# Kernel tuning notes

Hardware: AMD Instinct MI355X
Metric: run time of the kernel (lower is better)

Reference implementation:

```python
import jax, jax.numpy as jnp
import numpy as np

B, S, D = 128, 512, 768          # batch, seq_len, token_dim
NH, HD = 8, 96                    # num_heads, head_dim = sentence_dim/num_heads
HID = 4 * HD                      # hidden_dim = 384


def setup_inputs() -> dict:
    key = jax.random.key(0)
    ks = jax.random.split(key, 9)
    token_embeddings = jax.random.normal(ks[0], (B, S, D), dtype=jnp.float32)
    # variable-length attention mask (1 for real tokens, 0 for padding)
    lengths = jax.random.randint(ks[1], (B,), S // 2, S + 1)
    attention_mask = (jnp.arange(S)[None, :] < lengths[:, None]).astype(jnp.float32)
    s = 0.02
    P  = jax.random.normal(ks[2], (NH, HD, D),   dtype=jnp.float32) * s
    bP = jnp.zeros((NH, HD), dtype=jnp.float32)
    W1 = jax.random.normal(ks[3], (NH, HID, HD), dtype=jnp.float32) * s
    b1 = jnp.zeros((NH, HID), dtype=jnp.float32)
    W2 = jax.random.normal(ks[4], (NH, HD, HID), dtype=jnp.float32) * s
    b2 = jnp.zeros((NH, HD), dtype=jnp.float32)
    return {"token_embeddings": token_embeddings, "attention_mask": attention_mask,
            "P": P, "bP": bP, "W1": W1, "b1": b1, "W2": W2, "b2": b2}


def reference(token_embeddings, attention_mask, P, bP, W1, b1, W2, b2):
    # per-head projection: H_i = P_i(H)           -> (nh, B, S, HD)
    Hi = jnp.einsum('bsd,ihd->ibsh', token_embeddings, P) + bP[:, None, None, :]
    # scores: W2(relu(W1(H_i)))                   -> (nh, B, S, HD)
    A = jnp.einsum('ibsf,ihf->ibsh',
                   jax.nn.relu(jnp.einsum('ibsh,ifh->ibsf', Hi, W1) + b1[:, None, None, :]),
                   W2) + b2[:, None, None, :]
    # masked softmax over sequence dim (log(mask) adds -inf on padding)
    log_mask = jnp.log(attention_mask)[None, :, :, None]  # (1, B, S, 1)
    A = jax.nn.softmax(A + log_mask, axis=2)
    # weighted sum over tokens                    -> (nh, B, HD)
    v = jnp.sum(Hi * A, axis=2)
    # concat heads: (B, nh*HD) = (B, 768)
    pooled = jnp.transpose(v, (1, 0, 2)).reshape(token_embeddings.shape[0], NH * HD)
    return pooled
```

## Files before the change

### kernel.cpp

```cpp
#include <hip/hip_runtime.h>
#include <stdint.h>


typedef short bf16x8 __attribute__((ext_vector_type(8)));
typedef float f32x4 __attribute__((ext_vector_type(4)));

struct alignas(8) us4 { unsigned short x, y, z, w; };

__device__ __forceinline__ unsigned short f32_to_bf16(float f) {
  union { float f; uint32_t u; } v; v.f = f;
  uint32_t u = v.u;
  uint32_t r = (u + 0x7fffu + ((u >> 16) & 1u)) >> 16;
  return (unsigned short)r;
}

__device__ __forceinline__ float bf16_to_f32(unsigned short h) {
  union { uint32_t u; float f; } v; v.u = ((uint32_t)h) << 16;
  return v.f;
}

__device__ __forceinline__ uint32_t pack_bf16_trunc(float lo, float hi) {
  union { float f; uint32_t u; } a, b; a.f = lo; b.f = hi;
  return __builtin_amdgcn_perm(b.u, a.u, 0x07060302u);
}

__device__ __forceinline__ void g2l16(const unsigned short* g, unsigned short* l) {
  __builtin_amdgcn_global_load_lds((__attribute__((address_space(1))) void*)g,
                                   (__attribute__((address_space(3))) void*)l,
                                   16, 0, 0);
}

__device__ __forceinline__ void stageW(const unsigned short* __restrict__ src,
                                       unsigned short* dst, int w, int lane) {
#pragma unroll
  for (int it = 0; it < 4; ++it)
    g2l16(src + (size_t)((it * 4 + w) * 64 + lane) * 8, &dst[(it * 4 + w) * 512]);
  if (w < 2)
    g2l16(src + (size_t)((16 + w) * 64 + lane) * 8, &dst[(16 + w) * 512]);
}


#define N_X   50331648
#define N_P   589824
#define N_W1  294912
#define N_W2  294912
#define N_HI  50331648


__global__ __launch_bounds__(256) void prep(
    const float* __restrict__ X, const float* __restrict__ P,
    const float* __restrict__ W1, const float* __restrict__ W2,
    unsigned short* __restrict__ Xbf, unsigned short* __restrict__ Pbf,
    unsigned short* __restrict__ W1bf, unsigned short* __restrict__ W2bf) {
  const int bx = blockIdx.x;
  const int tid = threadIdx.x;
  if (bx < 49152) {
    const int idx = bx * 256 + tid;
    float4 v = ((const float4*)X)[idx];
    us4 o = {f32_to_bf16(v.x), f32_to_bf16(v.y), f32_to_bf16(v.z), f32_to_bf16(v.w)};
    ((us4*)Xbf)[idx] = o;
  } else if (bx < 49728) {
    const int idx = (bx - 49152) * 256 + tid;
    float4 v = ((const float4*)P)[idx];
    us4 o = {f32_to_bf16(v.x), f32_to_bf16(v.y), f32_to_bf16(v.z), f32_to_bf16(v.w)};
    ((us4*)Pbf)[idx] = o;
  } else if (bx < 49760) {
    const int quarter = bx - 49728;
    const int hd = quarter >> 2, ph = quarter & 3;
    for (int t = tid; t < 1152; t += 256) {
      const int kb = t / 384;
      const int rem = t - kb * 384;
      const int f = rem >> 2, slot = rem & 3;
      const int pos = slot ^ ((f >> 1) & 3);
      const float* src =
          W1 + ((size_t)(hd * 384 + ph * 96 + f)) * 96 + kb * 32 + pos * 8;
      float4 a = *(const float4*)src;
      float4 b = *(const float4*)(src + 4);
      us4 o1 = {f32_to_bf16(a.x), f32_to_bf16(a.y), f32_to_bf16(a.z), f32_to_bf16(a.w)};
      us4 o2 = {f32_to_bf16(b.x), f32_to_bf16(b.y), f32_to_bf16(b.z), f32_to_bf16(b.w)};
      us4* dst = (us4*)(W1bf + (size_t)quarter * 9216 + t * 8);
      dst[0] = o1;
      dst[1] = o2;
    }
  } else {
    const int quarter = bx - 49760;
    const int hd = quarter >> 2, ph = quarter & 3;
    for (int t = tid; t < 1152; t += 256) {
      const int kb = t / 384;
      const int rem = t - kb * 384;
      const int h = rem >> 2, slot = rem & 3;
      const int pos = slot ^ ((h >> 1) & 3);
      const float* src =
          W2 + ((size_t)(hd * 96 + h)) * 384 + ph * 96 + kb * 32 + pos * 8;
      float4 a = *(const float4*)src;
      float4 b = *(const float4*)(src + 4);
      us4 o1 = {f32_to_bf16(a.x), f32_to_bf16(a.y), f32_to_bf16(a.z), f32_to_bf16(a.w)};
      us4 o2 = {f32_to_bf16(b.x), f32_to_bf16(b.y), f32_to_bf16(b.z), f32_to_bf16(b.w)};
      us4* dst = (us4*)(W2bf + (size_t)quarter * 9216 + t * 8);
      dst[0] = o1;
      dst[1] = o2;
    }
  }
}


__global__ __launch_bounds__(256) void gemm_hi(
    const unsigned short* __restrict__ Xbf,
    const unsigned short* __restrict__ Pbf,
    const float* __restrict__ bP,
    unsigned short* __restrict__ Hi) {
  __shared__ __align__(16) unsigned short As[128 * 32];
  __shared__ __align__(16) unsigned short Bs[128 * 32];

  const int tid = threadIdx.x;
  const int w = tid >> 6;
  const int lane = tid & 63;
  const int r = lane & 15;
  const int q = lane >> 4;

  const int hwid = blockIdx.x;
  const int wkid = (hwid & 7) * 384 + (hwid >> 3);
  const int bn = wkid % 6;
  const int bm = wkid / 6;

  const int wr = w >> 1, wc = w & 1;
  const int psw = q ^ ((r >> 1) & 3);

  f32x4 acc[4][4];
#pragma unroll
  for (int a = 0; a < 4; ++a)
#pragma unroll
    for (int c = 0; c < 4; ++c) acc[a][c] = (f32x4){0.f, 0.f, 0.f, 0.f};

  const int ldr = lane >> 2;
  const int ldc = ((lane & 3) ^ ((lane >> 3) & 3)) * 8;
  const unsigned short* Abase = Xbf + (size_t)(bm * 128) * 768 + ldc;
  const unsigned short* Bbase = Pbf + (size_t)(bn * 128) * 768 + ldc;

  for (int k0 = 0; k0 < 768; k0 += 32) {
    __syncthreads();
    g2l16(Abase + (size_t)(w * 16 + ldr) * 768 + k0, &As[w * 512]);
    g2l16(Abase + (size_t)(64 + w * 16 + ldr) * 768 + k0, &As[(4 + w) * 512]);
    g2l16(Bbase + (size_t)(w * 16 + ldr) * 768 + k0, &Bs[w * 512]);
    g2l16(Bbase + (size_t)(64 + w * 16 + ldr) * 768 + k0, &Bs[(4 + w) * 512]);
    __syncthreads();

    bf16x8 af[4], bfr[4];
#pragma unroll
    for (int t = 0; t < 4; ++t)
      af[t] = *(const bf16x8*)&As[(wr * 64 + t * 16 + r) * 32 + psw * 8];
#pragma unroll
    for (int t = 0; t < 4; ++t)
      bfr[t] = *(const bf16x8*)&Bs[(wc * 64 + t * 16 + r) * 32 + psw * 8];
#pragma unroll
    for (int mt = 0; mt < 4; ++mt)
#pragma unroll
      for (int nt = 0; nt < 4; ++nt)
        acc[mt][nt] = __builtin_amdgcn_mfma_f32_16x16x32_bf16(
            af[mt], bfr[nt], acc[mt][nt], 0, 0, 0);
  }

  const int bb = bm >> 2;
  const int sb = (bm & 3) * 128 + wr * 64;
#pragma unroll
  for (int nt = 0; nt < 4; ++nt) {
    const int n0 = bn * 128 + wc * 64 + nt * 16;
    const int hd = n0 / 96;
    const int hloc = n0 - hd * 96;
    const int kb = hloc >> 5;
    const int col = (hloc & 31) + r;
    const float bias = bP[n0 + r];
    unsigned short* obase =
        Hi + (size_t)(hd * 128 + bb) * 49152 + kb * 16384 + col;
#pragma unroll
    for (int mt = 0; mt < 4; ++mt) {
#pragma unroll
      for (int rg = 0; rg < 4; ++rg) {
        const int s = sb + mt * 16 + q * 4 + rg;
        obase[(size_t)s * 32] = f32_to_bf16(acc[mt][nt][rg] + bias);
      }
    }
  }
}


__global__ __launch_bounds__(256, 3) void mlp_pool(
    const unsigned short* __restrict__ Hi,
    const unsigned short* __restrict__ W1bf,
    const unsigned short* __restrict__ W2bf,
    const float* __restrict__ b1,
    const float* __restrict__ b2,
    const float* __restrict__ mask,
    float* __restrict__ out) {
  __shared__ __align__(16) unsigned short U[128 * 104];
  __shared__ __align__(16) unsigned short Ws2[3 * 96 * 32];
  __shared__ __align__(16) float b1s[384];
  __shared__ __align__(16) float b2s[96];
  __shared__ float bias_s[512];
  __shared__ float redA[4][96];
  __shared__ float redB[4][96];

  const int x = blockIdx.x;
  const int b = x & 127;
  const int hd = x >> 7;

  const int tid = threadIdx.x;
  const int w = tid >> 6;
  const int lane = tid & 63;
  const int r = lane & 15;
  const int q = lane >> 4;
  const int psw = q ^ ((r >> 1) & 3);

  if (tid < 96) b2s[tid] = b2[hd * 96 + tid];
  for (int i = tid; i < 384; i += 256) b1s[i] = b1[hd * 384 + i];
  for (int s = tid; s < 512; s += 256)
    bias_s[s] = mask[b * 512 + s] > 0.5f ? 0.f : -1e30f;

  float m_run[6], l_run[6], v_run[6];
#pragma unroll
  for (int nt = 0; nt < 6; ++nt) { m_run[nt] = -3e30f; l_run[nt] = 0.f; v_run[nt] = 0.f; }

  const unsigned short* ysrc = Hi + (size_t)(hd * 128 + b) * 49152;
  const unsigned short* w1h = W1bf + (size_t)(hd * 4) * 9216;
  const unsigned short* w2h = W2bf + (size_t)(hd * 4) * 9216;

  for (int c = 0; c < 4; ++c) {
    const unsigned short* yc = ysrc + c * 4096;

    f32x4 acc3[2][6];
#pragma unroll
    for (int sp = 0; sp < 2; ++sp)
#pragma unroll
      for (int nt = 0; nt < 6; ++nt) acc3[sp][nt] = (f32x4){0.f, 0.f, 0.f, 0.f};

    for (int ph = 0; ph < 4; ++ph) {
      if (c | ph) __syncthreads();
      stageW(w1h + ph * 9216, U, w, lane);
      stageW(w2h + ph * 9216, Ws2, w, lane);
      __syncthreads();

      f32x4 acc2[6][2];
#pragma unroll
      for (int ft = 0; ft < 6; ++ft)
#pragma unroll
        for (int sp = 0; sp < 2; ++sp) acc2[ft][sp] = (f32x4){0.f, 0.f, 0.f, 0.f};
#pragma unroll
      for (int kb = 0; kb < 3; ++kb) {
        bf16x8 bfrg[2];
#pragma unroll
        for (int sp = 0; sp < 2; ++sp)
          bfrg[sp] = *(const bf16x8*)(yc + kb * 16384 +
                                      ((w * 2 + sp) * 16 + r) * 32 + q * 8);
#pragma unroll
        for (int ft = 0; ft < 6; ++ft) {
          bf16x8 afrg = *(const bf16x8*)&U[kb * 3072 + (ft * 16 + r) * 32 + psw * 8];
#pragma unroll
          for (int sp = 0; sp < 2; ++sp)
            acc2[ft][sp] = __builtin_amdgcn_mfma_f32_16x16x32_bf16(
                afrg, bfrg[sp], acc2[ft][sp], 0, 0, 0);
        }
      }
      __syncthreads();

#pragma unroll
      for (int ft = 0; ft < 6; ++ft) {
        float4 bv = *(const float4*)&b1s[ph * 96 + ft * 16 + q * 4];
#pragma unroll
        for (int sp = 0; sp < 2; ++sp) {
          const int s = (w * 2 + sp) * 16 + r;
          float v0 = fmaxf(acc2[ft][sp][0] + bv.x, 0.f);
          float v1 = fmaxf(acc2[ft][sp][1] + bv.y, 0.f);
          float v2 = fmaxf(acc2[ft][sp][2] + bv.z, 0.f);
          float v3 = fmaxf(acc2[ft][sp][3] + bv.w, 0.f);
          uint2 pk;
          pk.x = pack_bf16_trunc(v0, v1);
          pk.y = pack_bf16_trunc(v2, v3);
          *(uint2*)((uint32_t*)&U[0] + s * 52 + ft * 8 + q * 2) = pk;
        }
      }
      __syncthreads();

#pragma unroll
      for (int kb = 0; kb < 3; ++kb) {
        bf16x8 afrg[2];
#pragma unroll
        for (int sp = 0; sp < 2; ++sp)
          afrg[sp] = *(const bf16x8*)&U[((w * 2 + sp) * 16 + r) * 104 + kb * 32 + q * 8];
#pragma unroll
        for (int nt = 0; nt < 6; ++nt) {
          bf16x8 bfrg2 = *(const bf16x8*)&Ws2[kb * 3072 + (nt * 16 + r) * 32 + psw * 8];
#pragma unroll
          for (int sp = 0; sp < 2; ++sp)
            acc3[sp][nt] = __builtin_amdgcn_mfma_f32_16x16x32_bf16(
                afrg[sp], bfrg2, acc3[sp][nt], 0, 0, 0);
        }
      }
    }

#pragma unroll
    for (int nt = 0; nt < 6; ++nt) {
      const float b2v = b2s[nt * 16 + r];
      float lm = -3e30f;
#pragma unroll
      for (int sp = 0; sp < 2; ++sp) {
#pragma unroll
        for (int rg = 0; rg < 4; ++rg) {
          const int sl = (w * 2 + sp) * 16 + q * 4 + rg;
          float lg = acc3[sp][nt][rg] + b2v + bias_s[c * 128 + sl];
          lm = fmaxf(lm, lg);
        }
      }
      lm = fmaxf(lm, __shfl_xor(lm, 16));
      lm = fmaxf(lm, __shfl_xor(lm, 32));
      if (q == 0) redA[w][nt * 16 + r] = lm;
    }
    __syncthreads();
#pragma unroll
    for (int nt = 0; nt < 6; ++nt) {
      const int h = nt * 16 + r;
      const unsigned short* yb = yc + (nt >> 1) * 16384 + (nt & 1) * 16 + r;
      const float cm = fmaxf(fmaxf(redA[0][h], redA[1][h]),
                             fmaxf(redA[2][h], redA[3][h]));
      const float mnew = fmaxf(m_run[nt], cm);
      const float sc = __expf(m_run[nt] - mnew);
      m_run[nt] = mnew;
      float lacc = l_run[nt] * sc;
      float vacc = v_run[nt] * sc;
      const float b2v = b2s[h];
#pragma unroll
      for (int sp = 0; sp < 2; ++sp) {
#pragma unroll
        for (int rg = 0; rg < 4; ++rg) {
          const int sl = (w * 2 + sp) * 16 + q * 4 + rg;
          float lg = acc3[sp][nt][rg] + b2v + bias_s[c * 128 + sl];
          float e = __expf(lg - mnew);
          lacc += e;
          vacc += e * bf16_to_f32(yb[(size_t)sl * 32]);
        }
      }
      l_run[nt] = lacc;
      v_run[nt] = vacc;
    }
  }

  __syncthreads();
#pragma unroll
  for (int nt = 0; nt < 6; ++nt) {
    float ls = l_run[nt], vs = v_run[nt];
    ls += __shfl_xor(ls, 16);
    vs += __shfl_xor(vs, 16);
    ls += __shfl_xor(ls, 32);
    vs += __shfl_xor(vs, 32);
    if (q == 0) {
      redA[w][nt * 16 + r] = ls;
      redB[w][nt * 16 + r] = vs;
    }
  }
  __syncthreads();
  if (tid < 96) {
    float ls = redA[0][tid] + redA[1][tid] + redA[2][tid] + redA[3][tid];
    float vs = redB[0][tid] + redB[1][tid] + redB[2][tid] + redB[3][tid];
    out[(size_t)b * 768 + hd * 96 + tid] = vs / ls;
  }
}


extern "C" void kernel_launch(void* const* d_in, const int* in_sizes, int n_in,
                              void* d_out, int out_size, void* d_ws, size_t ws_size,
                              hipStream_t stream) {
  const float* X    = (const float*)d_in[0];
  const float* mask = (const float*)d_in[1];
  const float* P    = (const float*)d_in[2];
  const float* bP   = (const float*)d_in[3];
  const float* W1   = (const float*)d_in[4];
  const float* b1   = (const float*)d_in[5];
  const float* W2   = (const float*)d_in[6];
  const float* b2   = (const float*)d_in[7];
  float* out = (float*)d_out;
  (void)in_sizes; (void)n_in; (void)out_size; (void)ws_size;

  unsigned short* Xbf  = (unsigned short*)d_ws;
  unsigned short* Pbf  = Xbf + N_X;
  unsigned short* W1bf = Pbf + N_P;
  unsigned short* W2bf = W1bf + N_W1;
  unsigned short* Hi   = W2bf + N_W2;

  prep<<<49792, 256, 0, stream>>>(X, P, W1, W2, Xbf, Pbf, W1bf, W2bf);
  gemm_hi<<<3072, 256, 0, stream>>>(Xbf, Pbf, bP, Hi);
  mlp_pool<<<8 * 128, 256, 0, stream>>>(Hi, W1bf, W2bf, b1, b2, mask, out);
}
```

Before: 591.6 us.

## Stage Hi tiles in LDS and pass relu activations via lane shuffles

The token-chunk tile of Hi is loaded once per chunk into a swizzled LDS buffer, using async global-to-LDS copies. The first GEMM and the weighted value sum then read it from LDS rather than issuing scattered global loads. The intermediate relu activations are repacked into MFMA A-fragments with cross-lane shuffles instead of a round trip through shared memory. W1 and W2 now share one LDS buffer, staged one after the other with an extra barrier. Occupancy drops from 3 to 2 blocks per CU in exchange for more registers.

```diff
diff --git a/kernel.cpp b/kernel.cpp
--- a/kernel.cpp
+++ b/kernel.cpp
@@ -184,7 +184,7 @@
 }
 
 
-__global__ __launch_bounds__(256, 3) void mlp_pool(
+__global__ __launch_bounds__(256, 2) void mlp_pool(
     const unsigned short* __restrict__ Hi,
     const unsigned short* __restrict__ W1bf,
     const unsigned short* __restrict__ W2bf,
@@ -192,8 +192,8 @@
     const float* __restrict__ b2,
     const float* __restrict__ mask,
     float* __restrict__ out) {
-  __shared__ __align__(16) unsigned short U[128 * 104];
-  __shared__ __align__(16) unsigned short Ws2[3 * 96 * 32];
+  __shared__ __align__(16) unsigned short Ys[3 * 128 * 32];
+  __shared__ __align__(16) unsigned short Ws[96 * 96];
   __shared__ __align__(16) float b1s[384];
   __shared__ __align__(16) float b2s[96];
   __shared__ float bias_s[512];
@@ -210,6 +210,10 @@
   const int r = lane & 15;
   const int q = lane >> 4;
   const int psw = q ^ ((r >> 1) & 3);
+  const int ysx = (tid ^ ((tid >> 3) & 3)) * 8;
+  const int ra = r + ((q & 1) << 5);
+  const int rb = ra + 16;
+  const bool qhi = q >= 2;
 
   if (tid < 96) b2s[tid] = b2[hd * 96 + tid];
   for (int i = tid; i < 384; i += 256) b1s[i] = b1[hd * 384 + i];
@@ -225,7 +229,17 @@
   const unsigned short* w2h = W2bf + (size_t)(hd * 4) * 9216;
 
   for (int c = 0; c < 4; ++c) {
-    const unsigned short* yc = ysrc + c * 4096;
+    __syncthreads();
+
+    {
+      const unsigned short* yc0 = ysrc + c * 4096 + ysx;
+      g2l16(yc0, &Ys[w * 512]);
+      g2l16(yc0 + 2048, &Ys[(4 + w) * 512]);
+      g2l16(yc0 + 16384, &Ys[(8 + w) * 512]);
+      g2l16(yc0 + 18432, &Ys[(12 + w) * 512]);
+      g2l16(yc0 + 32768, &Ys[(16 + w) * 512]);
+      g2l16(yc0 + 34816, &Ys[(20 + w) * 512]);
+    }
 
     f32x4 acc3[2][6];
 #pragma unroll
@@ -234,9 +248,9 @@
       for (int nt = 0; nt < 6; ++nt) acc3[sp][nt] = (f32x4){0.f, 0.f, 0.f, 0.f};
 
     for (int ph = 0; ph < 4; ++ph) {
-      if (c | ph) __syncthreads();
-      stageW(w1h + ph * 9216, U, w, lane);
-      stageW(w2h + ph * 9216, Ws2, w, lane);
+      if (ph) __syncthreads();
+
+      stageW(w1h + ph * 9216, Ws, w, lane);
       __syncthreads();
 
       f32x4 acc2[6][2];
@@ -249,50 +263,66 @@
         bf16x8 bfrg[2];
 #pragma unroll
         for (int sp = 0; sp < 2; ++sp)
-          bfrg[sp] = *(const bf16x8*)(yc + kb * 16384 +
-                                      ((w * 2 + sp) * 16 + r) * 32 + q * 8);
+          bfrg[sp] = *(const bf16x8*)&Ys[kb * 4096 + ((w * 2 + sp) * 16 + r) * 32 + psw * 8];
 #pragma unroll
         for (int ft = 0; ft < 6; ++ft) {
-          bf16x8 afrg = *(const bf16x8*)&U[kb * 3072 + (ft * 16 + r) * 32 + psw * 8];
+          bf16x8 afrg = *(const bf16x8*)&Ws[kb * 3072 + (ft * 16 + r) * 32 + psw * 8];
 #pragma unroll
           for (int sp = 0; sp < 2; ++sp)
             acc2[ft][sp] = __builtin_amdgcn_mfma_f32_16x16x32_bf16(
                 afrg, bfrg[sp], acc2[ft][sp], 0, 0, 0);
         }
       }
-      __syncthreads();
-
+
+      uint32_t pkw0[6][2], pkw1[6][2];
 #pragma unroll
       for (int ft = 0; ft < 6; ++ft) {
         float4 bv = *(const float4*)&b1s[ph * 96 + ft * 16 + q * 4];
 #pragma unroll
         for (int sp = 0; sp < 2; ++sp) {
-          const int s = (w * 2 + sp) * 16 + r;
           float v0 = fmaxf(acc2[ft][sp][0] + bv.x, 0.f);
           float v1 = fmaxf(acc2[ft][sp][1] + bv.y, 0.f);
           float v2 = fmaxf(acc2[ft][sp][2] + bv.z, 0.f);
           float v3 = fmaxf(acc2[ft][sp][3] + bv.w, 0.f);
-          uint2 pk;
-          pk.x = pack_bf16_trunc(v0, v1);
-          pk.y = pack_bf16_trunc(v2, v3);
-          *(uint2*)((uint32_t*)&U[0] + s * 52 + ft * 8 + q * 2) = pk;
+          pkw0[ft][sp] = pack_bf16_trunc(v0, v1);
+          pkw1[ft][sp] = pack_bf16_trunc(v2, v3);
+        }
+      }
+      bf16x8 af_r[3][2];
+#pragma unroll
+      for (int kb = 0; kb < 3; ++kb) {
+#pragma unroll
+        for (int sp = 0; sp < 2; ++sp) {
+          uint32_t a0 = __shfl(pkw0[2 * kb][sp], ra);
+          uint32_t a1 = __shfl(pkw1[2 * kb][sp], ra);
+          uint32_t a2 = __shfl(pkw0[2 * kb][sp], rb);
+          uint32_t a3 = __shfl(pkw1[2 * kb][sp], rb);
+          uint32_t c0 = __shfl(pkw0[2 * kb + 1][sp], ra);
+          uint32_t c1 = __shfl(pkw1[2 * kb + 1][sp], ra);
+          uint32_t c2 = __shfl(pkw0[2 * kb + 1][sp], rb);
+          uint32_t c3 = __shfl(pkw1[2 * kb + 1][sp], rb);
+          union { uint32_t u[4]; bf16x8 v; } fu;
+          fu.u[0] = qhi ? c0 : a0;
+          fu.u[1] = qhi ? c1 : a1;
+          fu.u[2] = qhi ? c2 : a2;
+          fu.u[3] = qhi ? c3 : a3;
+          af_r[kb][sp] = fu.v;
         }
       }
       __syncthreads();
 
+      stageW(w2h + ph * 9216, Ws, w, lane);
+      __syncthreads();
+
 #pragma unroll
       for (int kb = 0; kb < 3; ++kb) {
-        bf16x8 afrg[2];
-#pragma unroll
-        for (int sp = 0; sp < 2; ++sp)
-          afrg[sp] = *(const bf16x8*)&U[((w * 2 + sp) * 16 + r) * 104 + kb * 32 + q * 8];
 #pragma unroll
         for (int nt = 0; nt < 6; ++nt) {
-          bf16x8 bfrg2 = *(const bf16x8*)&Ws2[kb * 3072 + (nt * 16 + r) * 32 + psw * 8];
+          bf16x8 bfrg2 = *(const bf16x8*)&Ws[kb * 3072 + (nt * 16 + r) * 32 + psw * 8];
 #pragma unroll
           for (int sp = 0; sp < 2; ++sp)
             acc3[sp][nt] = __builtin_amdgcn_mfma_f32_16x16x32_bf16(
-                afrg[sp], bfrg2, acc3[sp][nt], 0, 0, 0);
+                af_r[kb][sp], bfrg2, acc3[sp][nt], 0, 0, 0);
         }
       }
     }
@@ -318,7 +348,9 @@
 #pragma unroll
     for (int nt = 0; nt < 6; ++nt) {
       const int h = nt * 16 + r;
-      const unsigned short* yb = yc + (nt >> 1) * 16384 + (nt & 1) * 16 + r;
+      const int kbh = nt >> 1;
+      const int gh = (nt * 2 + (r >> 3)) & 3;
+      const int hlo = r & 7;
       const float cm = fmaxf(fmaxf(redA[0][h], redA[1][h]),
                              fmaxf(redA[2][h], redA[3][h]));
       const float mnew = fmaxf(m_run[nt], cm);
@@ -335,7 +367,8 @@
           float lg = acc3[sp][nt][rg] + b2v + bias_s[c * 128 + sl];
           float e = __expf(lg - mnew);
           lacc += e;
-          vacc += e * bf16_to_f32(yb[(size_t)sl * 32]);
+          const int pos = gh ^ ((sl >> 1) & 3);
+          vacc += e * bf16_to_f32(Ys[kbh * 4096 + sl * 32 + pos * 8 + hlo]);
         }
       }
       l_run[nt] = lacc;
```

Result: faster. 539.2 us (-8.9%).
